# Optimization experiments

Measured on AMD Instinct MI355X. Metric: run time of the kernel, lower is better.

The kernel has to match this reference:

```python
import jax, jax.numpy as jnp
import numpy as np

D = 1024  # input_size
NORM = 1.0 / np.sqrt(D)


def setup_inputs() -> dict:
    key = jax.random.key(0)
    k_x, k_q, k_k, k_v = jax.random.split(key, 4)
    B, S = 4, 2048
    scale = 1.0 / np.sqrt(D)  # init ~ nn.Linear default magnitude
    return {
        "inputs": jax.random.normal(k_x, (B, S, D), dtype=jnp.float32),
        "Wq": jax.random.uniform(k_q, (D, D), jnp.float32, -scale, scale),
        "Wk": jax.random.uniform(k_k, (D, D), jnp.float32, -scale, scale),
        "Wv": jax.random.uniform(k_v, (D, D), jnp.float32, -scale, scale),
    }


def reference(inputs, Wq, Wk, Wv):
    # nn.Linear(x) = x @ W.T (no bias)
    Q = jnp.einsum("bsd,ed->bse", inputs, Wq)
    K = jnp.einsum("bsd,ed->bse", inputs, Wk)
    V = jnp.einsum("bsd,ed->bse", inputs, Wv)
    attn = jnp.einsum("bqe,bke->bqk", Q, K) * NORM  # [B,S,S]
    attn = jax.nn.softmax(attn, axis=2)
    return jnp.einsum("bqk,bke->bqe", attn, V)
```

## Files before the change

### kernel.cpp

```cpp
#include <hip/hip_runtime.h>

typedef __bf16 bf16_t;
typedef __bf16 bf16x8 __attribute__((ext_vector_type(8)));
typedef __bf16 bf16x4 __attribute__((ext_vector_type(4)));
typedef float  floatx4 __attribute__((ext_vector_type(4)));

__device__ __forceinline__ void gload_lds16(const bf16_t* g, bf16_t* l) {
    __builtin_amdgcn_global_load_lds(
        (const __attribute__((address_space(1))) void*)g,
        (__attribute__((address_space(3))) void*)l,
        16, 0, 0);
}

template <int MODE, int BN, int MAP, typename OutT>
__global__ __launch_bounds__(512, 2) void gemm8p(
    const bf16_t* __restrict__ A, int lda, size_t batchA,
    const bf16_t* __restrict__ B, int ldb, size_t batchB,
    OutT* __restrict__ C, int ldc, size_t batchC,
    bf16_t* __restrict__ C2,
    float* __restrict__ rowsums, int batchR,
    int K, float scale)
{
    extern __shared__ __align__(16) bf16_t smem[];

    constexpr int NJ   = BN / 64;
    constexpr int WCB  = BN / 4;
    constexpr int BGL  = BN / 128;
    constexpr int AREG = 8192;
    constexpr int BREG = BN * 32;
    constexpr int BOFF = 2 * AREG;
    constexpr int BUFS = BOFF + 2 * BREG;
    constexpr int VM   = 2 + 2 * BGL;

    int bxL, byL, bzL;
    if constexpr (MAP == 1) {
        const int h = blockIdx.x, k = h & 7, s = h >> 3;
        bzL = k >> 1; bxL = ((k & 1) << 2) | (s & 3); byL = s >> 2;
    } else if constexpr (MAP == 2) {
        const int h = blockIdx.x, k = h & 7, s = h >> 3;
        bzL = 0; bxL = s >> 3; byL = (k << 3) | (s & 7);
    } else {
        bxL = blockIdx.x; byL = blockIdx.y; bzL = blockIdx.z;
    }

    A += (size_t)bzL * batchA;
    B += (size_t)bzL * batchB;

    const int tid  = threadIdx.x;
    const int wid  = tid >> 6;
    const int lane = tid & 63;
    const int wr   = wid >> 2;
    const int wc   = wid & 3;
    const int lr   = lane & 15;

    const int bm = bxL * 256;
    const int bn = byL * BN;

    const bf16_t* At = A + (size_t)bm * lda;
    const bf16_t* Bt = B + (size_t)bn * ldb;

    const int    c8 = (((lane & 3) ^ ((lane >> 3) & 3)) << 3);
    const size_t ga = (size_t)(wid * 16 + (lane >> 2)) * lda + c8;
    const size_t gb = (size_t)(wid * 16 + (lane >> 2)) * ldb + c8;

    const int slotoff = (((lane >> 4) ^ ((lr >> 1) & 3)) << 3);

    const int NT = K >> 6;

    floatx4 acc[8][NJ] = {};
    bf16x8 af[4], bq[NJ];

#define RBASE(sbuf, sreg)                                                     \
    ((sbuf) * BUFS + ((sreg) < 2 ? (sreg) * AREG : BOFF + ((sreg) - 2) * BREG))

#define STAGE(sbuf, sreg, tile) do {                                          \
    bf16_t* _l = smem + RBASE(sbuf, sreg) + (wid << 9);                       \
    const size_t _k = (size_t)(tile) * 64 + ((sreg) & 1) * 32;                \
    if ((sreg) >= 2) {                                                        \
        gload_lds16(Bt + _k + gb, _l);                                        \
        if (BGL == 2)                                                         \
            gload_lds16(Bt + _k + gb + (size_t)128 * ldb, _l + 4096);         \
    } else {                                                                  \
        gload_lds16(At + _k + ga, _l);                                        \
        gload_lds16(At + _k + ga + (size_t)128 * lda, _l + 4096);             \
    }                                                                         \
} while (0)

#define LDA_FRAG(buf, kk, row)                                                \
    (*(const bf16x8*)&smem[(buf) * BUFS + (kk) * AREG + ((row) << 5) + slotoff])
#define LDB_FRAG(buf, kk, row)                                                \
    (*(const bf16x8*)&smem[(buf) * BUFS + BOFF + (kk) * BREG + ((row) << 5) + slotoff])

#define PHASE(buf, kk, mh, RDB, sbuf, sreg, stile, DOVM) do {                 \
    if (RDB) {                                                                \
        _Pragma("unroll")                                                     \
        for (int j = 0; j < NJ; ++j)                                          \
            bq[j] = LDB_FRAG(buf, kk, wc * WCB + j * 16 + lr);                \
    }                                                                         \
    _Pragma("unroll")                                                         \
    for (int i = 0; i < 4; ++i)                                               \
        af[i] = LDA_FRAG(buf, kk, wr * 128 + (mh) * 64 + i * 16 + lr);        \
    STAGE(sbuf, sreg, stile);                                                 \
    if (DOVM) {                                                               \
        if constexpr (VM == 6) asm volatile("s_waitcnt vmcnt(6)" ::: "memory");\
        else                   asm volatile("s_waitcnt vmcnt(4)" ::: "memory");\
    }                                                                         \
    __builtin_amdgcn_s_barrier();                                             \
    __builtin_amdgcn_s_setprio(1);                                            \
    _Pragma("unroll")                                                         \
    for (int i = 0; i < 4; ++i) {                                             \
        _Pragma("unroll")                                                     \
        for (int j = 0; j < NJ; ++j)                                          \
            acc[(mh) * 4 + i][j] = __builtin_amdgcn_mfma_f32_16x16x32_bf16(   \
                bq[j], af[i], acc[(mh) * 4 + i][j], 0, 0, 0);                 \
    }                                                                         \
    __builtin_amdgcn_s_setprio(0);                                            \
    __builtin_amdgcn_s_barrier();                                             \
} while (0)

    STAGE(0, 2, 0); STAGE(0, 0, 0); STAGE(0, 3, 0); STAGE(0, 1, 0);
    STAGE(1, 2, 1); STAGE(1, 0, 1); STAGE(1, 3, 1);
    if constexpr (VM == 6) asm volatile("s_waitcnt vmcnt(6)" ::: "memory");
    else                   asm volatile("s_waitcnt vmcnt(4)" ::: "memory");
    __builtin_amdgcn_s_barrier();

    for (int kt = 0; kt < NT; kt += 2) {
        int t1 = kt + 1;
        int t2 = kt + 2; if (t2 >= NT) t2 -= NT;
        int t3 = kt + 3; if (t3 >= NT) t3 -= NT;
        PHASE(0, 0, 0, true,  1, 1, t1, false);
        PHASE(0, 0, 1, false, 0, 2, t2, false);
        PHASE(0, 1, 0, true,  0, 0, t2, false);
        PHASE(0, 1, 1, false, 0, 3, t2, true);
        PHASE(1, 0, 0, true,  0, 1, t2, false);
        PHASE(1, 0, 1, false, 1, 2, t3, false);
        PHASE(1, 1, 0, true,  1, 0, t3, false);
        PHASE(1, 1, 1, false, 1, 3, t3, true);
    }
    asm volatile("s_waitcnt vmcnt(0)" ::: "memory");

#undef PHASE
#undef LDA_FRAG
#undef LDB_FRAG
#undef STAGE
#undef RBASE

    const int cfix = lane & 15;
    const int creg = (lane >> 4) << 2;

    if constexpr (MODE == 1) {
        OutT* Cz = C + (size_t)bzL * batchC;
        #pragma unroll
        for (int mi = 0; mi < 8; ++mi) {
            size_t row = (size_t)(bm + wr * 128 + mi * 16 + cfix);
            #pragma unroll
            for (int j = 0; j < NJ; ++j) {
                int col = bn + wc * WCB + j * 16 + creg;
                bf16x4 v;
                #pragma unroll
                for (int r = 0; r < 4; ++r) v[r] = (bf16_t)acc[mi][j][r];
                *(bf16x4*)&Cz[row * (size_t)ldc + col] = v;
            }
        }
    } else if constexpr (MODE == 5) {
        bf16_t* dst = (bn < 1024) ? (bf16_t*)C : C2;
        const int cb = bn & 1023;
        #pragma unroll
        for (int mi = 0; mi < 8; ++mi) {
            size_t row = (size_t)(bm + wr * 128 + mi * 16 + cfix);
            #pragma unroll
            for (int j = 0; j < NJ; ++j) {
                int col = cb + wc * WCB + j * 16 + creg;
                bf16x4 v;
                #pragma unroll
                for (int r = 0; r < 4; ++r) v[r] = (bf16_t)acc[mi][j][r];
                *(bf16x4*)&dst[row * (size_t)ldc + col] = v;
            }
        }
    } else if constexpr (MODE == 2) {
        OutT* Cz = C + (size_t)bzL * batchC;
        float* sums = rowsums + (size_t)bzL * batchR;
        float rs[8] = {};
        #pragma unroll
        for (int mi = 0; mi < 8; ++mi) {
            size_t row = (size_t)(bm + wr * 128 + mi * 16 + cfix);
            #pragma unroll
            for (int j = 0; j < NJ; ++j) {
                int col = bn + wc * WCB + j * 16 + creg;
                bf16x4 v;
                #pragma unroll
                for (int r = 0; r < 4; ++r) {
                    v[r] = (bf16_t)__expf(acc[mi][j][r] * scale);
                    rs[mi] += (float)v[r];
                }
                *(bf16x4*)&Cz[row * (size_t)ldc + col] = v;
            }
        }
        #pragma unroll
        for (int mi = 0; mi < 8; ++mi) {
            rs[mi] += __shfl_xor(rs[mi], 16);
            rs[mi] += __shfl_xor(rs[mi], 32);
        }
        if (lane < 16) {
            #pragma unroll
            for (int mi = 0; mi < 8; ++mi)
                atomicAdd(&sums[bm + wr * 128 + mi * 16 + lane], rs[mi]);
        }
    } else {
        OutT* Cz = C + (size_t)bzL * batchC;
        const float* sums = rowsums + (size_t)bzL * batchR;
        #pragma unroll
        for (int mi = 0; mi < 8; ++mi) {
            int rloc = bm + wr * 128 + mi * 16 + cfix;
            float rinv = 1.0f / sums[rloc];
            size_t row = (size_t)rloc;
            #pragma unroll
            for (int j = 0; j < NJ; ++j) {
                int col = bn + wc * WCB + j * 16 + creg;
                floatx4 v;
                #pragma unroll
                for (int r = 0; r < 4; ++r) v[r] = acc[mi][j][r] * rinv;
                *(floatx4*)&Cz[row * (size_t)ldc + col] = v;
            }
        }
    }
}

__global__ __launch_bounds__(256) void cvt_all(
    const float* __restrict__ X, const float* __restrict__ Wq,
    const float* __restrict__ Wk, const float* __restrict__ Wv,
    bf16_t* __restrict__ Xb, bf16_t* __restrict__ Wqb,
    bf16_t* __restrict__ Wkb, bf16_t* __restrict__ Wvb,
    float* __restrict__ sums, int nsums,
    int nX4, int nW4)
{
    int i = blockIdx.x * blockDim.x + threadIdx.x;
    if (i < nsums) sums[i] = 0.f;
    const float* src; bf16_t* dst; int idx;
    if (i < nX4) { src = X; dst = Xb; idx = i; }
    else {
        int j = i - nX4;
        int w = j / nW4;
        idx = j - w * nW4;
        if (i >= nX4 + 3 * nW4) return;
        src = (w == 0) ? Wq : (w == 1) ? Wk : Wv;
        dst = (w == 0) ? Wqb : (w == 1) ? Wkb : Wvb;
    }
    float4 v = ((const float4*)src)[idx];
    bf16x4 o;
    o[0] = (bf16_t)v.x; o[1] = (bf16_t)v.y; o[2] = (bf16_t)v.z; o[3] = (bf16_t)v.w;
    *(bf16x4*)(dst + (size_t)idx * 4) = o;
}

extern "C" void kernel_launch(void* const* d_in, const int* in_sizes, int n_in,
                              void* d_out, int out_size, void* d_ws, size_t ws_size,
                              hipStream_t stream)
{
    (void)in_sizes; (void)n_in; (void)out_size; (void)ws_size;
    const float* X  = (const float*)d_in[0];
    const float* Wq = (const float*)d_in[1];
    const float* Wk = (const float*)d_in[2];
    const float* Wv = (const float*)d_in[3];
    float* out = (float*)d_out;

    const int Bb = 4, S = 2048, D = 1024;
    const int M = Bb * S;

    char* ws = (char*)d_ws;
    size_t off = 0;
    auto carve = [&](size_t bytes) -> char* {
        char* p = ws + off;
        off += (bytes + 255) & ~(size_t)255;
        return p;
    };
    bf16_t* Xb  = (bf16_t*)carve((size_t)M * D * 2);
    bf16_t* Wqb = (bf16_t*)carve((size_t)D * D * 2);
    bf16_t* Wkb = (bf16_t*)carve((size_t)D * D * 2);
    bf16_t* Wvb = (bf16_t*)carve((size_t)D * D * 2);
    bf16_t* Qb  = (bf16_t*)carve((size_t)M * D * 2);
    bf16_t* Kb  = (bf16_t*)carve((size_t)M * D * 2);
    bf16_t* Vt  = (bf16_t*)carve((size_t)D * M * 2);
    bf16_t* Sc  = (bf16_t*)carve((size_t)Bb * S * S * 2);
    float*  sums = (float*)carve((size_t)M * 4);

    static bool s_attr = false;
    if (!s_attr) {
        (void)hipFuncSetAttribute(
            reinterpret_cast<const void*>(&gemm8p<5, 256, 0, bf16_t>),
            hipFuncAttributeMaxDynamicSharedMemorySize, 131072);
        (void)hipFuncSetAttribute(
            reinterpret_cast<const void*>(&gemm8p<2, 256, 1, bf16_t>),
            hipFuncAttributeMaxDynamicSharedMemorySize, 131072);
        (void)hipFuncSetAttribute(
            reinterpret_cast<const void*>(&gemm8p<1, 128, 2, bf16_t>),
            hipFuncAttributeMaxDynamicSharedMemorySize, 98304);
        (void)hipFuncSetAttribute(
            reinterpret_cast<const void*>(&gemm8p<3, 128, 1, float>),
            hipFuncAttributeMaxDynamicSharedMemorySize, 98304);
        s_attr = true;
    }

    const int nX4 = M * D / 4, nW4 = D * D / 4;
    const int tot4 = nX4 + 3 * nW4;
    cvt_all<<<(tot4 + 255) / 256, 256, 0, stream>>>(
        X, Wq, Wk, Wv, Xb, Wqb, Wkb, Wvb, sums, M, nX4, nW4);

    gemm8p<5, 256, 0, bf16_t><<<dim3(M / 256, (2 * D) / 256, 1), 512, 131072, stream>>>(
        Xb, D, 0, Wqb, D, 0, Qb, D, 0, Kb, nullptr, 0, D, 1.0f);

    gemm8p<1, 128, 2, bf16_t><<<dim3(256, 1, 1), 512, 98304, stream>>>(
        Wvb, D, 0, Xb, D, 0, Vt, M, 0, nullptr, nullptr, 0, D, 1.0f);

    gemm8p<2, 256, 1, bf16_t><<<dim3(256, 1, 1), 512, 131072, stream>>>(
        Qb, D, (size_t)S * D, Kb, D, (size_t)S * D, Sc, S, (size_t)S * S,
        nullptr, sums, S, D, 0.03125f);

    gemm8p<3, 128, 1, float><<<dim3(256, 1, 1), 512, 98304, stream>>>(
        Sc, S, (size_t)S * S, Vt, M, (size_t)S, out, D, (size_t)S * D,
        nullptr, sums, S, S, 1.0f);
}
```

Measured before the change: 233.4 us.

## Double-buffer LDS fragment registers to prefetch next phase during MFMA

Fragment registers for A and B are now double-buffered. Each phase issues the LDS reads for the next phase after the barrier and then runs MFMAs on the fragments loaded earlier, so LDS read latency overlaps with matrix math instead of preceding it. A prologue preloads the first fragments. This doubles the fragment register footprint, which under launch_bounds(512,2) may cause spills or pressure, and the last iteration's prefetch reads wrapped buffers.

```diff
diff --git a/kernel.cpp b/kernel.cpp
--- a/kernel.cpp
+++ b/kernel.cpp
@@ -68,7 +68,7 @@
     const int NT = K >> 6;
 
     floatx4 acc[8][NJ] = {};
-    bf16x8 af[4], bq[NJ];
+    bf16x8 af[2][4], bq[2][NJ];
 
 #define RBASE(sbuf, sreg)                                                     \
     ((sbuf) * BUFS + ((sreg) < 2 ? (sreg) * AREG : BOFF + ((sreg) - 2) * BREG))
@@ -91,28 +91,28 @@
 #define LDB_FRAG(buf, kk, row)                                                \
     (*(const bf16x8*)&smem[(buf) * BUFS + BOFF + (kk) * BREG + ((row) << 5) + slotoff])
 
-#define PHASE(buf, kk, mh, RDB, sbuf, sreg, stile, DOVM) do {                 \
-    if (RDB) {                                                                \
-        _Pragma("unroll")                                                     \
-        for (int j = 0; j < NJ; ++j)                                          \
-            bq[j] = LDB_FRAG(buf, kk, wc * WCB + j * 16 + lr);                \
-    }                                                                         \
-    _Pragma("unroll")                                                         \
-    for (int i = 0; i < 4; ++i)                                               \
-        af[i] = LDA_FRAG(buf, kk, wr * 128 + (mh) * 64 + i * 16 + lr);        \
+#define PHASE(cm, CA, CB, nb, nk, nm, NRDB, sbuf, sreg, stile, DOVM) do {     \
     STAGE(sbuf, sreg, stile);                                                 \
     if (DOVM) {                                                               \
         if constexpr (VM == 6) asm volatile("s_waitcnt vmcnt(6)" ::: "memory");\
         else                   asm volatile("s_waitcnt vmcnt(4)" ::: "memory");\
     }                                                                         \
     __builtin_amdgcn_s_barrier();                                             \
+    if (NRDB) {                                                               \
+        _Pragma("unroll")                                                     \
+        for (int j = 0; j < NJ; ++j)                                          \
+            bq[CB ^ 1][j] = LDB_FRAG(nb, nk, wc * WCB + j * 16 + lr);         \
+    }                                                                         \
+    _Pragma("unroll")                                                         \
+    for (int i = 0; i < 4; ++i)                                               \
+        af[CA ^ 1][i] = LDA_FRAG(nb, nk, wr * 128 + (nm) * 64 + i * 16 + lr); \
     __builtin_amdgcn_s_setprio(1);                                            \
     _Pragma("unroll")                                                         \
     for (int i = 0; i < 4; ++i) {                                             \
         _Pragma("unroll")                                                     \
         for (int j = 0; j < NJ; ++j)                                          \
-            acc[(mh) * 4 + i][j] = __builtin_amdgcn_mfma_f32_16x16x32_bf16(   \
-                bq[j], af[i], acc[(mh) * 4 + i][j], 0, 0, 0);                 \
+            acc[(cm) * 4 + i][j] = __builtin_amdgcn_mfma_f32_16x16x32_bf16(   \
+                bq[CB][j], af[CA][i], acc[(cm) * 4 + i][j], 0, 0, 0);         \
     }                                                                         \
     __builtin_amdgcn_s_setprio(0);                                            \
     __builtin_amdgcn_s_barrier();                                             \
@@ -123,19 +123,25 @@
     if constexpr (VM == 6) asm volatile("s_waitcnt vmcnt(6)" ::: "memory");
     else                   asm volatile("s_waitcnt vmcnt(4)" ::: "memory");
     __builtin_amdgcn_s_barrier();
+    #pragma unroll
+    for (int j = 0; j < NJ; ++j)
+        bq[0][j] = LDB_FRAG(0, 0, wc * WCB + j * 16 + lr);
+    #pragma unroll
+    for (int i = 0; i < 4; ++i)
+        af[0][i] = LDA_FRAG(0, 0, wr * 128 + i * 16 + lr);
 
     for (int kt = 0; kt < NT; kt += 2) {
         int t1 = kt + 1;
         int t2 = kt + 2; if (t2 >= NT) t2 -= NT;
         int t3 = kt + 3; if (t3 >= NT) t3 -= NT;
-        PHASE(0, 0, 0, true,  1, 1, t1, false);
-        PHASE(0, 0, 1, false, 0, 2, t2, false);
-        PHASE(0, 1, 0, true,  0, 0, t2, false);
-        PHASE(0, 1, 1, false, 0, 3, t2, true);
-        PHASE(1, 0, 0, true,  0, 1, t2, false);
-        PHASE(1, 0, 1, false, 1, 2, t3, false);
-        PHASE(1, 1, 0, true,  1, 0, t3, false);
-        PHASE(1, 1, 1, false, 1, 3, t3, true);
+        PHASE(0, 0, 0,  0, 0, 1, 0,    1, 1, t1,  0);
+        PHASE(1, 1, 0,  0, 1, 0, 1,    0, 2, t2,  0);
+        PHASE(0, 0, 1,  0, 1, 1, 0,    0, 0, t2,  0);
+        PHASE(1, 1, 1,  1, 0, 0, 1,    0, 3, t2,  1);
+        PHASE(0, 0, 0,  1, 0, 1, 0,    0, 1, t2,  0);
+        PHASE(1, 1, 0,  1, 1, 0, 1,    1, 2, t3,  0);
+        PHASE(0, 0, 1,  1, 1, 1, 0,    1, 0, t3,  0);
+        PHASE(1, 1, 1,  0, 0, 0, 1,    1, 3, t3,  1);
     }
     asm volatile("s_waitcnt vmcnt(0)" ::: "memory");
 
```

Result: no change. 234.1 us (+0.3%).
